# Performance work log

Measured on AMD Instinct MI355X. Metric: run time of the kernel, lower is better.

The kernel has to match this reference:

```python
import jax, jax.numpy as jnp
import numpy as np

EPS = 1e-5

def _block(x, W, b, g, be):
    # Linear -> LayerNorm -> ReLU, fused elementwise chain
    h = x @ W + b
    mu = jnp.mean(h, axis=-1, keepdims=True)
    var = jnp.mean(jnp.square(h - mu), axis=-1, keepdims=True)
    hn = (h - mu) * jax.lax.rsqrt(var + EPS) * g + be
    return jnp.maximum(hn, 0.0)

def setup_inputs() -> dict:
    key = jax.random.key(0)
    ks = jax.random.split(key, 6)
    B, D_IN, H, D_OUT = 262144, 48, 256, 12
    s_in = 1.0 / np.sqrt(D_IN)
    s_h = 1.0 / np.sqrt(H)
    return {
        "x": jax.random.normal(ks[0], (B, D_IN), jnp.float32),
        "W1": jax.random.normal(ks[1], (D_IN, H), jnp.float32) * s_in,
        "b1": jnp.zeros((H,), jnp.float32),
        "g1": jnp.ones((H,), jnp.float32),
        "be1": jnp.zeros((H,), jnp.float32),
        "W2": jax.random.normal(ks[2], (H, H), jnp.float32) * s_h,
        "b2": jnp.zeros((H,), jnp.float32),
        "g2": jnp.ones((H,), jnp.float32),
        "be2": jnp.zeros((H,), jnp.float32),
        "W3": jax.random.normal(ks[3], (H, H), jnp.float32) * s_h,
        "b3": jnp.zeros((H,), jnp.float32),
        "g3": jnp.ones((H,), jnp.float32),
        "be3": jnp.zeros((H,), jnp.float32),
        "Wm": jax.random.normal(ks[4], (H, D_OUT), jnp.float32) * s_h,
        "bm": jnp.zeros((D_OUT,), jnp.float32),
    }

def reference(x, W1, b1, g1, be1, W2, b2, g2, be2, W3, b3, g3, be3, Wm, bm):
    h = _block(x, W1, b1, g1, be1)
    h = _block(h, W2, b2, g2, be2)
    h = _block(h, W3, b3, g3, be3)
    return jnp.tanh(h @ Wm + bm)
```

## Files before the change

kernel.cpp:

```cpp
#include <hip/hip_runtime.h>
#include <hip/hip_bf16.h>

#define BATCH 262144
#define DIN 48
#define HDIM 256
#define DOUT 12
#define EPSV 1e-5f

#define ROWS_PER_BLOCK 128
#define NBLK (BATCH / ROWS_PER_BLOCK)

typedef __attribute__((ext_vector_type(4))) float f32x4;
typedef __attribute__((ext_vector_type(8))) short bf16x8;

union FragU { bf16x8 v; unsigned u[4]; };

#define W1F_OFF 0
#define W2F_OFF 16384
#define W3F_OFF 81920
#define WMF_OFF 147456
#define WS_ELEMS 151552

__device__ __forceinline__ unsigned short f2b(float f) {
    union { float f; unsigned u; } v; v.f = f;
    unsigned r = (v.u + 0x7fffu + ((v.u >> 16) & 1u)) >> 16;
    return (unsigned short)r;
}

__device__ __forceinline__ unsigned packbf(float a, float b) {
    float2 t; t.x = a; t.y = b;
    __hip_bfloat162 h = __float22bfloat162_rn(t);
    union { __hip_bfloat162 h; unsigned u; } c; c.h = h;
    return c.u;
}

__global__ void conv_w_kernel(const float* __restrict__ W1, const float* __restrict__ b1,
                              const float* __restrict__ W2, const float* __restrict__ W3,
                              const float* __restrict__ Wm,
                              unsigned short* __restrict__ ws) {
    int i = blockIdx.x * 256 + threadIdx.x;
    if (i >= WS_ELEMS) return;
    float v;
    if (i < WMF_OFF) {
        int base, which;
        if (i < W2F_OFF)      { base = i - W1F_OFF; which = 0; }
        else if (i < W3F_OFF) { base = i - W2F_OFF; which = 1; }
        else                  { base = i - W3F_OFF; which = 2; }
        const int s = base >> 13;
        const int u = base & 8191;
        const int tid = u >> 5;
        const int h = (u >> 3) & 3;
        const int j = u & 7;
        const int fm = h * 2048 + tid * 8 + j;
        const int t = fm >> 9;
        const int l = (fm >> 3) & 63;
        const int jj = fm & 7;
        const int n = 16 * t + (l & 15);
        if (which == 0) {
            const int k = 32 * s + 8 * (l >> 4) + jj;
            v = (k < DIN) ? W1[k * HDIM + n] : (k == DIN ? b1[n] : 0.0f);
        } else {
            const int k = 32 * s + ((jj >= 4) ? 16 : 0) + 4 * (l >> 4) + (jj & 3);
            v = (which == 1) ? W2[k * HDIM + n] : W3[k * HDIM + n];
        }
    } else {
        const int i4 = i - WMF_OFF;
        const int j = i4 & 7, l = (i4 >> 3) & 63, ks = i4 >> 9;
        const int n = l & 15;
        const int k = 32 * ks + ((j >= 4) ? 16 : 0) + 4 * (l >> 4) + (j & 3);
        v = (n < DOUT) ? Wm[k * DOUT + n] : 0.0f;
    }
    ws[i] = f2b(v);
}

template<int KS>
__device__ __forceinline__ void mm_layer(
    f32x4 (&acc)[2][16], const FragU (&bf)[2][8],
    unsigned short (&slab)[2][8192], int& p,
    const unsigned short* __restrict__ wt, const unsigned short* __restrict__ wtnext,
    int tid, int lane)
{
    #pragma unroll
    for (int s = 0; s < KS; s++) {
        int4 R0, R1, R2, R3;
        const bool pf = (s + 1 < KS) || (wtnext != nullptr);
        if (s + 1 < KS) {
            const int4* g = (const int4*)(wt + (s + 1) * 8192 + tid * 32);
            R0 = g[0]; R1 = g[1]; R2 = g[2]; R3 = g[3];
        } else if (wtnext != nullptr) {
            const int4* g = (const int4*)(wtnext + tid * 32);
            R0 = g[0]; R1 = g[1]; R2 = g[2]; R3 = g[3];
        }
        __builtin_amdgcn_s_setprio(1);
        #pragma unroll
        for (int t = 0; t < 16; t++) {
            const bf16x8 A = *(const bf16x8*)&slab[p][(t * 64 + lane) * 8];
            acc[0][t] = __builtin_amdgcn_mfma_f32_16x16x32_bf16(A, bf[0][s].v, acc[0][t], 0, 0, 0);
            acc[1][t] = __builtin_amdgcn_mfma_f32_16x16x32_bf16(A, bf[1][s].v, acc[1][t], 0, 0, 0);
        }
        __builtin_amdgcn_s_setprio(0);
        if (pf) {
            unsigned short* sb = &slab[p ^ 1][0];
            *(int4*)&sb[tid * 8]        = R0;
            *(int4*)&sb[2048 + tid * 8] = R1;
            *(int4*)&sb[4096 + tid * 8] = R2;
            *(int4*)&sb[6144 + tid * 8] = R3;
        }
        __syncthreads();
        p ^= 1;
    }
}

__device__ __forceinline__ void build_frags(
    const f32x4 (&acc)[2][16], FragU (&bfo)[2][8],
    const float2* __restrict__ gbeL, int lane)
{
    const int q = lane >> 4;
    #pragma unroll
    for (int rt = 0; rt < 2; rt++) {
        float ss = 0.f, qq = 0.f;
        #pragma unroll
        for (int t = 0; t < 16; t++)
            #pragma unroll
            for (int r = 0; r < 4; r++) {
                const float v = acc[rt][t][r];
                ss += v; qq = fmaf(v, v, qq);
            }
        ss += __shfl_xor(ss, 16); ss += __shfl_xor(ss, 32);
        qq += __shfl_xor(qq, 16); qq += __shfl_xor(qq, 32);
        const float mu = ss * (1.0f / 256.0f);
        const float rs = rsqrtf(fmaxf(qq * (1.0f / 256.0f) - mu * mu, 0.0f) + EPSV);
        const float nb = -mu * rs;
        #pragma unroll
        for (int ks = 0; ks < 8; ks++) {
            const float4 a0 = *(const float4*)&gbeL[32 * ks + 4 * q];
            const float4 a1 = *(const float4*)&gbeL[32 * ks + 4 * q + 2];
            const float4 b0 = *(const float4*)&gbeL[32 * ks + 16 + 4 * q];
            const float4 b1 = *(const float4*)&gbeL[32 * ks + 16 + 4 * q + 2];
            float w00 = fmaxf(fmaf(fmaf(acc[rt][2 * ks][0], rs, nb), a0.x, a0.y), 0.f);
            float w01 = fmaxf(fmaf(fmaf(acc[rt][2 * ks][1], rs, nb), a0.z, a0.w), 0.f);
            float w02 = fmaxf(fmaf(fmaf(acc[rt][2 * ks][2], rs, nb), a1.x, a1.y), 0.f);
            float w03 = fmaxf(fmaf(fmaf(acc[rt][2 * ks][3], rs, nb), a1.z, a1.w), 0.f);
            float w10 = fmaxf(fmaf(fmaf(acc[rt][2 * ks + 1][0], rs, nb), b0.x, b0.y), 0.f);
            float w11 = fmaxf(fmaf(fmaf(acc[rt][2 * ks + 1][1], rs, nb), b0.z, b0.w), 0.f);
            float w12 = fmaxf(fmaf(fmaf(acc[rt][2 * ks + 1][2], rs, nb), b1.x, b1.y), 0.f);
            float w13 = fmaxf(fmaf(fmaf(acc[rt][2 * ks + 1][3], rs, nb), b1.z, b1.w), 0.f);
            bfo[rt][ks].u[0] = packbf(w00, w01);
            bfo[rt][ks].u[1] = packbf(w02, w03);
            bfo[rt][ks].u[2] = packbf(w10, w11);
            bfo[rt][ks].u[3] = packbf(w12, w13);
        }
    }
}

__device__ __forceinline__ void zero_acc(f32x4 (&acc)[2][16]) {
    #pragma unroll
    for (int rt = 0; rt < 2; rt++)
        #pragma unroll
        for (int t = 0; t < 16; t++)
            acc[rt][t] = (f32x4){0.f, 0.f, 0.f, 0.f};
}

__device__ __forceinline__ void init_acc_bias(f32x4 (&acc)[2][16],
                                              const float* __restrict__ bt, int q) {
    #pragma unroll
    for (int t = 0; t < 16; t++) {
        const float4 b = *(const float4*)&bt[16 * t + 4 * q];
        acc[0][t] = (f32x4){b.x, b.y, b.z, b.w};
        acc[1][t] = (f32x4){b.x, b.y, b.z, b.w};
    }
}

__global__ __launch_bounds__(256, 2) void fused_mlp(
    const float* __restrict__ x,
    const float* __restrict__ g1, const float* __restrict__ be1,
    const float* __restrict__ b2, const float* __restrict__ g2, const float* __restrict__ be2,
    const float* __restrict__ b3, const float* __restrict__ g3, const float* __restrict__ be3,
    const float* __restrict__ bm,
    const unsigned short* __restrict__ ws,
    float* __restrict__ out)
{
    __shared__ unsigned short slab[2][8192];
    __shared__ float2 gbe[3][256];
    __shared__ float btab[2][256];
    __shared__ float bmt[16];
    __shared__ float ostage[4][384];

    const int tid = threadIdx.x;
    const int wv = tid >> 6, lane = tid & 63;
    const int l15 = lane & 15, q = lane >> 4;
    const int wrow0 = blockIdx.x * ROWS_PER_BLOCK + wv * 32;

    const unsigned short* w1f = ws + W1F_OFF;
    const unsigned short* w2f = ws + W2F_OFF;
    const unsigned short* w3f = ws + W3F_OFF;
    const unsigned short* wmf = ws + WMF_OFF;

    {
        const int n = tid;
        gbe[0][n] = make_float2(g1[n], be1[n]);
        gbe[1][n] = make_float2(g2[n], be2[n]);
        gbe[2][n] = make_float2(g3[n], be3[n]);
        btab[0][n] = b2[n];
        btab[1][n] = b3[n];
        if (tid < 16) bmt[tid] = (tid < DOUT) ? bm[tid] : 0.f;
    }
    {
        const int4* g = (const int4*)(w1f + tid * 32);
        int4 r0 = g[0], r1 = g[1], r2 = g[2], r3 = g[3];
        unsigned short* sb = &slab[0][0];
        *(int4*)&sb[tid * 8]        = r0;
        *(int4*)&sb[2048 + tid * 8] = r1;
        *(int4*)&sb[4096 + tid * 8] = r2;
        *(int4*)&sb[6144 + tid * 8] = r3;
    }
    FragU bf[2][8];
    #pragma unroll
    for (int rt = 0; rt < 2; rt++) {
        const float* xr = x + (size_t)(wrow0 + rt * 16 + l15) * DIN;
        const float4 f0 = *(const float4*)(xr + q * 8);
        const float4 f1 = *(const float4*)(xr + q * 8 + 4);
        bf[rt][0].u[0] = packbf(f0.x, f0.y); bf[rt][0].u[1] = packbf(f0.z, f0.w);
        bf[rt][0].u[2] = packbf(f1.x, f1.y); bf[rt][0].u[3] = packbf(f1.z, f1.w);
        if (q < 2) {
            const float4 f2 = *(const float4*)(xr + 32 + q * 8);
            const float4 f3 = *(const float4*)(xr + 36 + q * 8);
            bf[rt][1].u[0] = packbf(f2.x, f2.y); bf[rt][1].u[1] = packbf(f2.z, f2.w);
            bf[rt][1].u[2] = packbf(f3.x, f3.y); bf[rt][1].u[3] = packbf(f3.z, f3.w);
        } else if (q == 2) {
            bf[rt][1].u[0] = 0x00003F80u;
            bf[rt][1].u[1] = 0u; bf[rt][1].u[2] = 0u; bf[rt][1].u[3] = 0u;
        } else {
            bf[rt][1].u[0] = 0u; bf[rt][1].u[1] = 0u;
            bf[rt][1].u[2] = 0u; bf[rt][1].u[3] = 0u;
        }
    }
    __syncthreads();

    f32x4 acc[2][16];
    int p = 0;

    zero_acc(acc);
    mm_layer<2>(acc, bf, slab, p, w1f, w2f, tid, lane);
    build_frags(acc, bf, &gbe[0][0], lane);

    init_acc_bias(acc, &btab[0][0], q);
    mm_layer<8>(acc, bf, slab, p, w2f, w3f, tid, lane);
    build_frags(acc, bf, &gbe[1][0], lane);

    init_acc_bias(acc, &btab[1][0], q);
    mm_layer<8>(acc, bf, slab, p, w3f, (const unsigned short*)nullptr, tid, lane);
    build_frags(acc, bf, &gbe[2][0], lane);

    f32x4 facc[2];
    {
        const float4 bm4 = *(const float4*)&bmt[4 * q];
        facc[0] = (f32x4){bm4.x, bm4.y, bm4.z, bm4.w};
        facc[1] = facc[0];
    }
    #pragma unroll
    for (int ks = 0; ks < 8; ks++) {
        const bf16x8 A = *(const bf16x8*)&wmf[(ks * 64 + lane) * 8];
        facc[0] = __builtin_amdgcn_mfma_f32_16x16x32_bf16(A, bf[0][ks].v, facc[0], 0, 0, 0);
        facc[1] = __builtin_amdgcn_mfma_f32_16x16x32_bf16(A, bf[1][ks].v, facc[1], 0, 0, 0);
    }
    if (q < 3) {
        #pragma unroll
        for (int rt = 0; rt < 2; rt++) {
            float4 o;
            o.x = tanhf(facc[rt][0]);
            o.y = tanhf(facc[rt][1]);
            o.z = tanhf(facc[rt][2]);
            o.w = tanhf(facc[rt][3]);
            *(float4*)&ostage[wv][(rt * 16 + l15) * 12 + q * 4] = o;
        }
    }
    float4* og = (float4*)(out + (size_t)wrow0 * DOUT);
    const float4* ov = (const float4*)&ostage[wv][0];
    og[lane] = ov[lane];
    if (lane < 32) og[64 + lane] = ov[64 + lane];
}

extern "C" void kernel_launch(void* const* d_in, const int* in_sizes, int n_in,
                              void* d_out, int out_size, void* d_ws, size_t ws_size,
                              hipStream_t stream)
{
    const float* x   = (const float*)d_in[0];
    const float* W1  = (const float*)d_in[1];
    const float* b1  = (const float*)d_in[2];
    const float* g1  = (const float*)d_in[3];
    const float* be1 = (const float*)d_in[4];
    const float* W2  = (const float*)d_in[5];
    const float* b2  = (const float*)d_in[6];
    const float* g2  = (const float*)d_in[7];
    const float* be2 = (const float*)d_in[8];
    const float* W3  = (const float*)d_in[9];
    const float* b3  = (const float*)d_in[10];
    const float* g3  = (const float*)d_in[11];
    const float* be3 = (const float*)d_in[12];
    const float* Wm  = (const float*)d_in[13];
    const float* bm  = (const float*)d_in[14];
    unsigned short* ws = (unsigned short*)d_ws;
    float* out = (float*)d_out;

    conv_w_kernel<<<(WS_ELEMS + 255) / 256, 256, 0, stream>>>(W1, b1, W2, W3, Wm, ws);
    fused_mlp<<<NBLK, 256, 0, stream>>>(x, g1, be1, b2, g2, be2,
                                        b3, g3, be3, bm, ws, out);
}
```

Baseline: 105.0 us.

## Stage weights via direct global-to-LDS loads in double-buffered slab pairs

```diff
diff --git a/kernel.cpp b/kernel.cpp
--- a/kernel.cpp
+++ b/kernel.cpp
@@ -32,6 +32,11 @@
     __hip_bfloat162 h = __float22bfloat162_rn(t);
     union { __hip_bfloat162 h; unsigned u; } c; c.h = h;
     return c.u;
+}
+
+__device__ __forceinline__ float fast_tanh(float x) {
+    const float t = __expf(2.0f * x);
+    return fmaf(-2.0f, __builtin_amdgcn_rcpf(t + 1.0f), 1.0f);
 }
 
 __global__ void conv_w_kernel(const float* __restrict__ W1, const float* __restrict__ b1,
@@ -41,28 +46,22 @@
     int i = blockIdx.x * 256 + threadIdx.x;
     if (i >= WS_ELEMS) return;
     float v;
-    if (i < WMF_OFF) {
-        int base, which;
-        if (i < W2F_OFF)      { base = i - W1F_OFF; which = 0; }
-        else if (i < W3F_OFF) { base = i - W2F_OFF; which = 1; }
-        else                  { base = i - W3F_OFF; which = 2; }
-        const int s = base >> 13;
-        const int u = base & 8191;
-        const int tid = u >> 5;
-        const int h = (u >> 3) & 3;
-        const int j = u & 7;
-        const int fm = h * 2048 + tid * 8 + j;
-        const int t = fm >> 9;
-        const int l = (fm >> 3) & 63;
-        const int jj = fm & 7;
+    if (i < W2F_OFF) {
+        const int j = i & 7, l = (i >> 3) & 63, t = (i >> 9) & 15, s = i >> 13;
+        const int n = 16 * t + (l & 15), k = 32 * s + 8 * (l >> 4) + j;
+        v = (k < DIN) ? W1[k * HDIM + n] : (k == DIN ? b1[n] : 0.0f);
+    } else if (i < W3F_OFF) {
+        const int i2 = i - W2F_OFF;
+        const int j = i2 & 7, l = (i2 >> 3) & 63, t = (i2 >> 9) & 15, s = i2 >> 13;
         const int n = 16 * t + (l & 15);
-        if (which == 0) {
-            const int k = 32 * s + 8 * (l >> 4) + jj;
-            v = (k < DIN) ? W1[k * HDIM + n] : (k == DIN ? b1[n] : 0.0f);
-        } else {
-            const int k = 32 * s + ((jj >= 4) ? 16 : 0) + 4 * (l >> 4) + (jj & 3);
-            v = (which == 1) ? W2[k * HDIM + n] : W3[k * HDIM + n];
-        }
+        const int k = 32 * s + ((j >= 4) ? 16 : 0) + 4 * (l >> 4) + (j & 3);
+        v = W2[k * HDIM + n];
+    } else if (i < WMF_OFF) {
+        const int i3 = i - W3F_OFF;
+        const int j = i3 & 7, l = (i3 >> 3) & 63, t = (i3 >> 9) & 15, s = i3 >> 13;
+        const int n = 16 * t + (l & 15);
+        const int k = 32 * s + ((j >= 4) ? 16 : 0) + 4 * (l >> 4) + (j & 3);
+        v = W3[k * HDIM + n];
     } else {
         const int i4 = i - WMF_OFF;
         const int j = i4 & 7, l = (i4 >> 3) & 63, ks = i4 >> 9;
@@ -73,39 +72,43 @@
     ws[i] = f2b(v);
 }
 
-template<int KS>
+__device__ __forceinline__ void gll16(const void* g, void* l) {
+    __builtin_amdgcn_global_load_lds(
+        (const __attribute__((address_space(1))) unsigned int*)g,
+        (__attribute__((address_space(3))) unsigned int*)l, 16, 0, 0);
+}
+
+__device__ __forceinline__ void stage_pair(const unsigned short* __restrict__ src,
+                                           unsigned short* dst, int tid) {
+    const char* g = (const char*)src + tid * 16;
+    char* l = (char*)dst + tid * 16;
+    #pragma unroll
+    for (int c = 0; c < 8; c++)
+        gll16(g + c * 4096, l + c * 4096);
+}
+
+template<int NP>
 __device__ __forceinline__ void mm_layer(
     f32x4 (&acc)[2][16], const FragU (&bf)[2][8],
-    unsigned short (&slab)[2][8192], int& p,
+    unsigned short (&buf)[2][16384], int& p,
     const unsigned short* __restrict__ wt, const unsigned short* __restrict__ wtnext,
     int tid, int lane)
 {
     #pragma unroll
-    for (int s = 0; s < KS; s++) {
-        int4 R0, R1, R2, R3;
-        const bool pf = (s + 1 < KS) || (wtnext != nullptr);
-        if (s + 1 < KS) {
-            const int4* g = (const int4*)(wt + (s + 1) * 8192 + tid * 32);
-            R0 = g[0]; R1 = g[1]; R2 = g[2]; R3 = g[3];
-        } else if (wtnext != nullptr) {
-            const int4* g = (const int4*)(wtnext + tid * 32);
-            R0 = g[0]; R1 = g[1]; R2 = g[2]; R3 = g[3];
-        }
+    for (int pp = 0; pp < NP; pp++) {
+        const unsigned short* nxt = (pp + 1 < NP) ? (wt + (pp + 1) * 16384) : wtnext;
+        if (nxt) stage_pair(nxt, &buf[p ^ 1][0], tid);
         __builtin_amdgcn_s_setprio(1);
         #pragma unroll
-        for (int t = 0; t < 16; t++) {
-            const bf16x8 A = *(const bf16x8*)&slab[p][(t * 64 + lane) * 8];
-            acc[0][t] = __builtin_amdgcn_mfma_f32_16x16x32_bf16(A, bf[0][s].v, acc[0][t], 0, 0, 0);
-            acc[1][t] = __builtin_amdgcn_mfma_f32_16x16x32_bf16(A, bf[1][s].v, acc[1][t], 0, 0, 0);
+        for (int h = 0; h < 2; h++) {
+            #pragma unroll
+            for (int t = 0; t < 16; t++) {
+                const bf16x8 A = *(const bf16x8*)&buf[p][h * 8192 + (t * 64 + lane) * 8];
+                acc[0][t] = __builtin_amdgcn_mfma_f32_16x16x32_bf16(A, bf[0][2 * pp + h].v, acc[0][t], 0, 0, 0);
+                acc[1][t] = __builtin_amdgcn_mfma_f32_16x16x32_bf16(A, bf[1][2 * pp + h].v, acc[1][t], 0, 0, 0);
+            }
         }
         __builtin_amdgcn_s_setprio(0);
-        if (pf) {
-            unsigned short* sb = &slab[p ^ 1][0];
-            *(int4*)&sb[tid * 8]        = R0;
-            *(int4*)&sb[2048 + tid * 8] = R1;
-            *(int4*)&sb[4096 + tid * 8] = R2;
-            *(int4*)&sb[6144 + tid * 8] = R3;
-        }
         __syncthreads();
         p ^= 1;
     }
@@ -129,7 +132,8 @@
         ss += __shfl_xor(ss, 16); ss += __shfl_xor(ss, 32);
         qq += __shfl_xor(qq, 16); qq += __shfl_xor(qq, 32);
         const float mu = ss * (1.0f / 256.0f);
-        const float rs = rsqrtf(fmaxf(qq * (1.0f / 256.0f) - mu * mu, 0.0f) + EPSV);
+        const float rs = __builtin_amdgcn_rsqf(
+            fmaxf(qq * (1.0f / 256.0f) - mu * mu, 0.0f) + EPSV);
         const float nb = -mu * rs;
         #pragma unroll
         for (int ks = 0; ks < 8; ks++) {
@@ -180,7 +184,7 @@
     const unsigned short* __restrict__ ws,
     float* __restrict__ out)
 {
-    __shared__ unsigned short slab[2][8192];
+    __shared__ unsigned short buf[2][16384];
     __shared__ float2 gbe[3][256];
     __shared__ float btab[2][256];
     __shared__ float bmt[16];
@@ -196,6 +200,7 @@
     const unsigned short* w3f = ws + W3F_OFF;
     const unsigned short* wmf = ws + WMF_OFF;
 
+    stage_pair(w1f, &buf[0][0], tid);
     {
         const int n = tid;
         gbe[0][n] = make_float2(g1[n], be1[n]);
@@ -204,15 +209,6 @@
         btab[0][n] = b2[n];
         btab[1][n] = b3[n];
         if (tid < 16) bmt[tid] = (tid < DOUT) ? bm[tid] : 0.f;
-    }
-    {
-        const int4* g = (const int4*)(w1f + tid * 32);
-        int4 r0 = g[0], r1 = g[1], r2 = g[2], r3 = g[3];
-        unsigned short* sb = &slab[0][0];
-        *(int4*)&sb[tid * 8]        = r0;
-        *(int4*)&sb[2048 + tid * 8] = r1;
-        *(int4*)&sb[4096 + tid * 8] = r2;
-        *(int4*)&sb[6144 + tid * 8] = r3;
     }
     FragU bf[2][8];
     #pragma unroll
@@ -241,15 +237,15 @@
     int p = 0;
 
     zero_acc(acc);
-    mm_layer<2>(acc, bf, slab, p, w1f, w2f, tid, lane);
+    mm_layer<1>(acc, bf, buf, p, w1f, w2f, tid, lane);
     build_frags(acc, bf, &gbe[0][0], lane);
 
     init_acc_bias(acc, &btab[0][0], q);
-    mm_layer<8>(acc, bf, slab, p, w2f, w3f, tid, lane);
+    mm_layer<4>(acc, bf, buf, p, w2f, w3f, tid, lane);
     build_frags(acc, bf, &gbe[1][0], lane);
 
     init_acc_bias(acc, &btab[1][0], q);
-    mm_layer<8>(acc, bf, slab, p, w3f, (const unsigned short*)nullptr, tid, lane);
+    mm_layer<4>(acc, bf, buf, p, w3f, (const unsigned short*)nullptr, tid, lane);
     build_frags(acc, bf, &gbe[2][0], lane);
 
     f32x4 facc[2];
@@ -268,10 +264,10 @@
         #pragma unroll
         for (int rt = 0; rt < 2; rt++) {
             float4 o;
-            o.x = tanhf(facc[rt][0]);
-            o.y = tanhf(facc[rt][1]);
-            o.z = tanhf(facc[rt][2]);
-            o.w = tanhf(facc[rt][3]);
+            o.x = fast_tanh(facc[rt][0]);
+            o.y = fast_tanh(facc[rt][1]);
+            o.z = fast_tanh(facc[rt][2]);
+            o.w = fast_tanh(facc[rt][3]);
             *(float4*)&ostage[wv][(rt * 16 + l15) * 12 + q * 4] = o;
         }
     }
```

Result: no change. 103.0 us (-1.9%).
